# Kernel tuning notes

Measured on AMD Instinct MI355X. Metric: run time of the kernel, lower is better.

## Reference

```python
import jax, jax.numpy as jnp
import numpy as np


def _hippo_dplr(n):
    # HiPPO-LegS -> NPLR -> DPLR (diagonal plus low rank) init, as in S4
    pr = np.sqrt(1.0 + 2.0 * np.arange(n))
    A = -(np.tril(pr[:, None] * pr[None, :]) - np.diag(np.arange(n)))
    p = np.sqrt(np.arange(n) + 0.5)
    b = np.sqrt(2.0 * np.arange(n) + 1.0)
    S = A + p[:, None] * p[None, :]
    lam_re = np.full(n, np.mean(np.diagonal(S)))
    lam_im, V = np.linalg.eigh(S * -1j)  # S*-1j is Hermitian
    p_c = V.conj().T @ p.astype(np.complex128)
    b_c = V.conj().T @ b.astype(np.complex128)
    return lam_re, lam_im, p_c, b_c


def setup_inputs():
    B, L, H, N = 4, 1024, 512, 64
    key = jax.random.key(0)
    kx, kc, ks, k1, k2 = jax.random.split(key, 5)
    lam_re, lam_im, p_c, b_c = _hippo_dplr(N)
    c = jax.random.normal(kc, (N, 2)) * (0.5 ** 0.5)
    f32 = lambda a: jnp.asarray(a, dtype=jnp.float32)
    return {
        'x': jax.random.normal(kx, (B, L, H), dtype=jnp.float32),
        'norm_weight': jnp.ones((H,), jnp.float32),
        'norm_bias': jnp.zeros((H,), jnp.float32),
        'lambda_re': f32(lam_re), 'lambda_im': f32(lam_im),
        'p_re': f32(p_c.real), 'p_im': f32(p_c.imag),
        'b_re': f32(b_c.real), 'b_im': f32(b_c.imag),
        'c_re': c[:, 0].astype(jnp.float32), 'c_im': c[:, 1].astype(jnp.float32),
        'd': jnp.ones((), jnp.float32),
        'log_step': jax.random.uniform(ks, (), jnp.float32, float(np.log(0.001)), float(np.log(0.1))),
        'out_w': (jax.random.normal(k1, (H, H), jnp.float32) / np.sqrt(H)).astype(jnp.float32),
        'out_b': jnp.zeros((H,), jnp.float32),
        'out2_w': (jax.random.normal(k2, (H, H), jnp.float32) / np.sqrt(H)).astype(jnp.float32),
        'out2_b': jnp.zeros((H,), jnp.float32),
    }


def reference(x, norm_weight, norm_bias, lambda_re, lambda_im, p_re, p_im,
              b_re, b_im, c_re, c_im, d, log_step, out_w, out_b, out2_w, out2_b):
    Bsz, L, H = x.shape
    skip = x
    # LayerNorm over channel dim (eps=1e-5, eqx default)
    mu = jnp.mean(x, -1, keepdims=True)
    var = jnp.mean((x - mu) ** 2, -1, keepdims=True)
    xn = (x - mu) / jnp.sqrt(var + 1e-5) * norm_weight + norm_bias
    # --- S4 DPLR bilinear discretization ---
    lam = (lambda_re + 1j * lambda_im).astype(jnp.complex64)
    p = (p_re + 1j * p_im).astype(jnp.complex64)
    b = (b_re + 1j * b_im).astype(jnp.complex64)
    c = (c_re + 1j * c_im).astype(jnp.complex64)
    step = jnp.exp(log_step).astype(jnp.complex64)
    N = lam.shape[0]
    I = jnp.eye(N, dtype=jnp.complex64)
    A = jnp.diag(lam) - p[:, None] * p[None, :].conj()
    A0 = (2.0 / step) * I + A
    Dinv = jnp.diag(1.0 / ((2.0 / step) - lam))
    qcD = p.conj()[None, :] @ Dinv           # [1,N]
    Dp = Dinv @ p[:, None]                   # [N,1]
    A1 = Dinv - (Dp @ qcD) / (1.0 + (qcD @ p[:, None]))  # Woodbury
    Ab = A1 @ A0                             # [N,N] discrete state matrix
    Bb = 2.0 * (A1 @ b[:, None])[:, 0]       # [N]
    # --- sequential state-space scan over time, vectorized over (B,H) lanes ---
    u = xn.astype(jnp.complex64)             # [B,L,H]

    def step_fn(state, u_t):                 # state: [B,H,N], u_t: [B,H]
        new = jnp.einsum('nm,bhm->bhn', Ab, state) + u_t[..., None] * Bb
        return new, jnp.einsum('n,bhn->bh', c, new).real

    init = jnp.zeros((Bsz, H, N), jnp.complex64)
    _, ys = jax.lax.scan(step_fn, init, jnp.moveaxis(u, 1, 0))  # ys: [L,B,H]
    y = jnp.moveaxis(ys, 0, 1) + d * xn      # feedthrough term
    # --- GELU + GLU-style gated output projection, residual ---
    y = jax.nn.gelu(y)
    gate = jax.nn.sigmoid(y @ out2_w.T + out2_b)
    return skip + (y @ out_w.T + out_b) * gate
```

## Files before the change

kernel.cpp:

```cpp
#include <hip/hip_runtime.h>
#include <hip/hip_bf16.h>
#include <math.h>

#define HDIM 512
#define LSEQ 1024
#define BSZ  4

typedef __attribute__((ext_vector_type(8))) short short8;
typedef __attribute__((ext_vector_type(4))) float floatx4;

__device__ __forceinline__ float2 cmul(float2 a, float2 b) {
  float2 r;
  r.x = a.x * b.x - a.y * b.y;
  r.y = a.x * b.y + a.y * b.x;
  return r;
}
__device__ __forceinline__ float2 cadd(float2 a, float2 b) {
  float2 r; r.x = a.x + b.x; r.y = a.y + b.y; return r;
}
__device__ __forceinline__ float2 cfma(float2 a, float2 b, float2 c) {
  c.x += a.x * b.x - a.y * b.y;
  c.y += a.x * b.y + a.y * b.x;
  return c;
}
__device__ __forceinline__ ushort f2bf(float f) {
  __hip_bfloat16 h = __float2bfloat16(f);
  return *(ushort*)&h;
}
__device__ __forceinline__ float bf2f(ushort u) {
  return __bfloat162float(*(__hip_bfloat16*)&u);
}

__global__ __launch_bounds__(576) void stage1_kernel(
    const float* __restrict__ x, const float* __restrict__ nw,
    const float* __restrict__ nb, float* __restrict__ xn,
    const float* __restrict__ lre, const float* __restrict__ lim,
    const float* __restrict__ pre, const float* __restrict__ pim,
    const float* __restrict__ bre, const float* __restrict__ bim,
    const float* __restrict__ cre, const float* __restrict__ cim,
    const float* __restrict__ logstep, float* __restrict__ Kout,
    const float* __restrict__ w1, const float* __restrict__ w2,
    ushort* __restrict__ Wst) {
  __shared__ float2 Ldab[64], Lu[64], Lr[64], LBb[64];
  __shared__ float2 Rv[2048];
  __shared__ float2 Wv[2048];
  int tid = threadIdx.x;
  int wv = tid >> 6;
  int lane = tid & 63;

  if (blockIdx.x != 0) {
    int row = (blockIdx.x - 1) * 9 + wv;
    if (row < BSZ * LSEQ) {
      const float* xr = x + (size_t)row * HDIM;
      float4 v0 = ((const float4*)xr)[lane];
      float4 v1 = ((const float4*)xr)[lane + 64];
      float s  = v0.x + v0.y + v0.z + v0.w + v1.x + v1.y + v1.z + v1.w;
      float ss = v0.x*v0.x + v0.y*v0.y + v0.z*v0.z + v0.w*v0.w
               + v1.x*v1.x + v1.y*v1.y + v1.z*v1.z + v1.w*v1.w;
      #pragma unroll
      for (int m = 1; m < 64; m <<= 1) { s += __shfl_xor(s, m); ss += __shfl_xor(ss, m); }
      float mu   = s * (1.0f / HDIM);
      float var  = ss * (1.0f / HDIM) - mu * mu;
      float rstd = rsqrtf(var + 1e-5f);
      float4 w0 = ((const float4*)nw)[lane];
      float4 w1v = ((const float4*)nw)[lane + 64];
      float4 b0 = ((const float4*)nb)[lane];
      float4 b1 = ((const float4*)nb)[lane + 64];
      float4 o0, o1;
      o0.x = (v0.x - mu) * rstd * w0.x + b0.x;
      o0.y = (v0.y - mu) * rstd * w0.y + b0.y;
      o0.z = (v0.z - mu) * rstd * w0.z + b0.z;
      o0.w = (v0.w - mu) * rstd * w0.w + b0.w;
      o1.x = (v1.x - mu) * rstd * w1v.x + b1.x;
      o1.y = (v1.y - mu) * rstd * w1v.y + b1.y;
      o1.z = (v1.z - mu) * rstd * w1v.z + b1.z;
      o1.w = (v1.w - mu) * rstd * w1v.w + b1.w;
      float* xo = xn + (size_t)row * HDIM;
      ((float4*)xo)[lane] = o0;
      ((float4*)xo)[lane + 64] = o1;
    }
    int idx = (blockIdx.x - 1) * 576 + tid;
    if (idx < 65536) {
      int e0 = idx * 8;
      int n = e0 >> 9, k0 = e0 & 511;
      const float* Wr = (n < 512) ? (w1 + (size_t)n * 512 + k0)
                                  : (w2 + (size_t)(n - 512) * 512 + k0);
      ushort tmp[8];
      #pragma unroll
      for (int q = 0; q < 8; q++) tmp[q] = f2bf(Wr[q]);
      *(short8*)&Wst[e0] = *(short8*)tmp;
    }
    return;
  }

  if (tid < 64) {
    int n = tid;
    float step = expf(logstep[0]);
    float g = 2.0f / step;
    float lr = lre[n], li = lim[n];
    float pr = pre[n], pi = pim[n];
    float br = bre[n], bi = bim[n];
    float den  = (g - lr) * (g - lr) + li * li;
    float dinr = (g - lr) / den, dini = li / den;
    float dabr = (g + lr) * dinr - li * dini;
    float dabi = (g + lr) * dini + li * dinr;
    float ur = dinr * pr - dini * pi;
    float ui = dinr * pi + dini * pr;
    float qr = pr * dinr + pi * dini;
    float qi = pr * dini - pi * dinr;
    float pm2 = pr * pr + pi * pi;
    float betr = pm2 * dinr, beti = pm2 * dini;
    float gar = qr * br - qi * bi;
    float gai = qr * bi + qi * br;
    #pragma unroll
    for (int m = 1; m < 64; m <<= 1) {
      betr += __shfl_xor(betr, m); beti += __shfl_xor(beti, m);
      gar  += __shfl_xor(gar, m);  gai  += __shfl_xor(gai, m);
    }
    float obr = 1.0f + betr, obi = beti;
    float ob2 = obr * obr + obi * obi;
    float kr = -2.0f * g * obr / ob2;
    float ki =  2.0f * g * obi / ob2;
    float rr = kr * qr - ki * qi;
    float ri = kr * qi + ki * qr;
    float tgr = (gar * obr + gai * obi) / ob2;
    float tgi = (gai * obr - gar * obi) / ob2;
    float dbr = dinr * br - dini * bi;
    float dbi = dinr * bi + dini * br;
    float Bbr = 2.0f * (dbr - (ur * tgr - ui * tgi));
    float Bbi = 2.0f * (dbi - (ur * tgi + ui * tgr));
    float2 t;
    t.x = dabr; t.y = dabi; Ldab[n] = t;
    t.x = ur;   t.y = ui;   Lu[n]   = t;
    t.x = rr;   t.y = ri;   Lr[n]   = t;
    t.x = Bbr;  t.y = Bbi;  LBb[n]  = t;
  }
  if (wv == 8) { float2 cc; cc.x = cre[lane]; cc.y = cim[lane]; Rv[lane] = cc; }
  __syncthreads();

  int g8 = lane >> 3;
  int q8 = lane & 7;
  int jm = wv * 8 + g8;
  float2 cv[8];

  if (wv < 8) {
    float2 dab[8], u[8], rn[8];
    #pragma unroll
    for (int ii = 0; ii < 8; ii++) {
      int n = q8 * 8 + ii;
      dab[ii] = Ldab[n]; u[ii] = Lu[n]; rn[ii] = Lr[n];
    }
    float2 rj = Lr[jm];
    #pragma unroll
    for (int ii = 0; ii < 8; ii++) {
      int n = q8 * 8 + ii;
      cv[ii] = cmul(u[ii], rj);
      if (n == jm) cv[ii] = cadd(cv[ii], dab[ii]);
    }
    for (int s = 0; s < 31; s++) {
      float2 part; part.x = 0.f; part.y = 0.f;
      #pragma unroll
      for (int ii = 0; ii < 8; ii++) part = cfma(rn[ii], cv[ii], part);
      #pragma unroll
      for (int m = 1; m < 8; m <<= 1) {
        part.x += __shfl_xor(part.x, m);
        part.y += __shfl_xor(part.y, m);
      }
      #pragma unroll
      for (int ii = 0; ii < 8; ii++) {
        float2 nc = cmul(dab[ii], cv[ii]);
        cv[ii] = cfma(u[ii], part, nc);
      }
    }
  } else {
    float2 dab0 = Ldab[lane], u0 = Lu[lane], r0 = Lr[lane];
    float2 w = LBb[lane];
    Wv[lane * 32 + 0] = w;
    for (int b = 1; b < 32; b++) {
      float dr = r0.x * w.x - r0.y * w.y;
      float di = r0.x * w.y + r0.y * w.x;
      #pragma unroll
      for (int m = 1; m < 64; m <<= 1) { dr += __shfl_xor(dr, m); di += __shfl_xor(di, m); }
      float2 nw2;
      nw2.x = dab0.x * w.x - dab0.y * w.y + u0.x * dr - u0.y * di;
      nw2.y = dab0.x * w.y + dab0.y * w.x + u0.x * di + u0.y * dr;
      w = nw2;
      Wv[lane * 32 + b] = w;
    }
  }
  __syncthreads();

  for (int a = 1; a < 32; a++) {
    if (wv < 8) {
      float2 part; part.x = 0.f; part.y = 0.f;
      #pragma unroll
      for (int ii = 0; ii < 8; ii++) {
        float2 Rk = Rv[(a - 1) * 64 + q8 * 8 + ii];
        part = cfma(Rk, cv[ii], part);
      }
      #pragma unroll
      for (int m = 1; m < 8; m <<= 1) {
        part.x += __shfl_xor(part.x, m);
        part.y += __shfl_xor(part.y, m);
      }
      if (q8 == 0) Rv[a * 64 + jm] = part;
    }
    __syncthreads();
  }

  for (int midx = tid; midx < 1024; midx += 576) {
    int a = midx >> 5, b = midx & 31;
    float acc = 0.f;
    for (int n = 0; n < 64; n++) {
      float2 R = Rv[a * 64 + n];
      float2 W = Wv[n * 32 + b];
      acc += R.x * W.x - R.y * W.y;
    }
    Kout[midx] = acc;
  }
}

__global__ __launch_bounds__(256) void conv_gemm_kernel(
    const float* __restrict__ K, const float* __restrict__ xn,
    const float* __restrict__ dptr, __hip_bfloat16* __restrict__ A) {
  __shared__ ushort sbuf[2 * 7680];
  int tid = threadIdx.x;
  int lane = tid & 63;
  int wv = tid >> 6;
  int wm = wv >> 1, wn = wv & 1;
  int by = blockIdx.y;
  int bm = (by < 8) ? by : 23 - by;
  int bn = blockIdx.x;
  floatx4 acc[2][2] = {};
  int srow = tid >> 2;
  int scol = (tid & 3) * 8;
  int ldst = srow * 40 + scol;
  int fr = lane & 15, fq = (lane >> 4) * 8;
  int trow = bm * 64 + srow;
  int tbase = trow - scol;
  int c = bn * 64 + srow;
  const float* xrow = xn + ((size_t)(c >> 9) * LSEQ) * HDIM + (c & 511);
  int KT = 2 * (bm + 1);

  float tv[8], uv[8];
  #pragma unroll
  for (int i = 0; i < 8; i++) {
    int idx = tbase - i;
    tv[i] = (idx >= 0) ? K[idx] : 0.f;
    uv[i] = xrow[(size_t)(scol + i) * HDIM];
  }
  {
    ushort th[8], tl[8], uu[8];
    #pragma unroll
    for (int i = 0; i < 8; i++) {
      th[i] = f2bf(tv[i]);
      tl[i] = f2bf(tv[i] - bf2f(th[i]));
      uu[i] = f2bf(uv[i]);
    }
    *(short8*)&sbuf[ldst]        = *(short8*)th;
    *(short8*)&sbuf[ldst + 2560] = *(short8*)tl;
    *(short8*)&sbuf[ldst + 5120] = *(short8*)uu;
  }
  __syncthreads();
  for (int kt = 0; kt < KT; kt++) {
    int cur = kt & 1;
    if (kt + 1 < KT) {
      int k0 = (kt + 1) * 32;
      #pragma unroll
      for (int i = 0; i < 8; i++) {
        int idx = tbase - k0 - i;
        tv[i] = (idx >= 0) ? K[idx] : 0.f;
        uv[i] = xrow[(size_t)(k0 + scol + i) * HDIM];
      }
    }
    const ushort* sTh = sbuf + cur * 7680;
    const ushort* sTl = sTh + 2560;
    const ushort* sUh = sTh + 5120;
    short8 ah[2], al[2], bh[2];
    #pragma unroll
    for (int i = 0; i < 2; i++) {
      ah[i] = *(const short8*)&sTh[(wm * 32 + i * 16 + fr) * 40 + fq];
      al[i] = *(const short8*)&sTl[(wm * 32 + i * 16 + fr) * 40 + fq];
      bh[i] = *(const short8*)&sUh[(wn * 32 + i * 16 + fr) * 40 + fq];
    }
    #pragma unroll
    for (int i = 0; i < 2; i++)
      #pragma unroll
      for (int j = 0; j < 2; j++) {
        acc[i][j] = __builtin_amdgcn_mfma_f32_16x16x32_bf16(ah[i], bh[j], acc[i][j], 0, 0, 0);
        acc[i][j] = __builtin_amdgcn_mfma_f32_16x16x32_bf16(al[i], bh[j], acc[i][j], 0, 0, 0);
      }
    if (kt + 1 < KT) {
      ushort th[8], tl[8], uu[8];
      #pragma unroll
      for (int i = 0; i < 8; i++) {
        th[i] = f2bf(tv[i]);
        tl[i] = f2bf(tv[i] - bf2f(th[i]));
        uu[i] = f2bf(uv[i]);
      }
      ushort* dst = sbuf + (cur ^ 1) * 7680;
      *(short8*)&dst[ldst]        = *(short8*)th;
      *(short8*)&dst[ldst + 2560] = *(short8*)tl;
      *(short8*)&dst[ldst + 5120] = *(short8*)uu;
      __syncthreads();
    }
  }
  float d = dptr[0];
  int row0 = bm * 64 + wm * 32;
  int col0 = bn * 64 + wn * 32;
  int fc = lane & 15, frq = (lane >> 4) * 4;
  #pragma unroll
  for (int i = 0; i < 2; i++)
    #pragma unroll
    for (int j = 0; j < 2; j++)
      #pragma unroll
      for (int r = 0; r < 4; r++) {
        int t = row0 + i * 16 + frq + r;
        int cc = col0 + j * 16 + fc;
        int b = cc >> 9, h = cc & 511;
        size_t off = (size_t)(b * LSEQ + t) * HDIM + h;
        float y = acc[i][j][r] + d * xn[off];
        float tnh = tanhf(0.7978845608028654f * (y + 0.044715f * y * y * y));
        A[off] = __float2bfloat16(0.5f * y * (1.0f + tnh));
      }
}

__global__ __launch_bounds__(256) void proj_kernel(
    const __hip_bfloat16* __restrict__ Abuf, const ushort* __restrict__ Wst,
    const float* __restrict__ x, const float* __restrict__ ob,
    const float* __restrict__ o2b, float* __restrict__ out) {
  __shared__ ushort sbuf[2 * 7680];
  int tid = threadIdx.x;
  int lane = tid & 63;
  int wv = tid >> 6;
  int wm = wv >> 1, wn = wv & 1;
  int bm = blockIdx.y, bn = blockIdx.x;
  int srow = tid >> 2;
  int scol = (tid & 3) * 8;
  int ldst = srow * 40 + scol;
  int fr = lane & 15, fq = (lane >> 4) * 8;
  floatx4 acc1[2][2] = {}, acc2[2][2] = {};
  const ushort* Ab = (const ushort*)Abuf;
  size_t Aoff  = (size_t)(bm * 64 + srow) * 512 + scol;
  size_t W1off = (size_t)(bn * 64 + srow) * 512 + scol;
  size_t W2off = W1off + (size_t)512 * 512;
  {
    uint4 a0 = *(const uint4*)&Ab[Aoff];
    uint4 v1 = *(const uint4*)&Wst[W1off];
    uint4 v2 = *(const uint4*)&Wst[W2off];
    *(uint4*)&sbuf[ldst]        = a0;
    *(uint4*)&sbuf[ldst + 2560] = v1;
    *(uint4*)&sbuf[ldst + 5120] = v2;
  }
  __syncthreads();
  for (int kt = 0; kt < 16; kt++) {
    int cur = kt & 1;
    uint4 na = {}, n1 = {}, n2 = {};
    if (kt + 1 < 16) {
      int k1 = (kt + 1) * 32;
      na = *(const uint4*)&Ab[Aoff + k1];
      n1 = *(const uint4*)&Wst[W1off + k1];
      n2 = *(const uint4*)&Wst[W2off + k1];
    }
    const ushort* sA  = sbuf + cur * 7680;
    const ushort* sW1 = sA + 2560;
    const ushort* sW2 = sA + 5120;
    short8 af[2], b1[2], b2[2];
    #pragma unroll
    for (int i = 0; i < 2; i++) {
      af[i] = *(const short8*)&sA[(wm * 32 + i * 16 + fr) * 40 + fq];
      b1[i] = *(const short8*)&sW1[(wn * 32 + i * 16 + fr) * 40 + fq];
      b2[i] = *(const short8*)&sW2[(wn * 32 + i * 16 + fr) * 40 + fq];
    }
    #pragma unroll
    for (int i = 0; i < 2; i++)
      #pragma unroll
      for (int j = 0; j < 2; j++) {
        acc1[i][j] = __builtin_amdgcn_mfma_f32_16x16x32_bf16(af[i], b1[j], acc1[i][j], 0, 0, 0);
        acc2[i][j] = __builtin_amdgcn_mfma_f32_16x16x32_bf16(af[i], b2[j], acc2[i][j], 0, 0, 0);
      }
    if (kt + 1 < 16) {
      ushort* dst = sbuf + (cur ^ 1) * 7680;
      *(uint4*)&dst[ldst]        = na;
      *(uint4*)&dst[ldst + 2560] = n1;
      *(uint4*)&dst[ldst + 5120] = n2;
      __syncthreads();
    }
  }
  int row0 = bm * 64 + wm * 32;
  int col0 = bn * 64 + wn * 32;
  int fc = lane & 15, frq = (lane >> 4) * 4;
  #pragma unroll
  for (int i = 0; i < 2; i++)
    #pragma unroll
    for (int j = 0; j < 2; j++)
      #pragma unroll
      for (int r = 0; r < 4; r++) {
        int row = row0 + i * 16 + frq + r;
        int col = col0 + j * 16 + fc;
        float c1 = acc1[i][j][r] + ob[col];
        float c2 = acc2[i][j][r] + o2b[col];
        float gate = 1.0f / (1.0f + expf(-c2));
        size_t off = (size_t)row * HDIM + col;
        out[off] = x[off] + c1 * gate;
      }
}

extern "C" void kernel_launch(void* const* d_in, const int* in_sizes, int n_in,
                              void* d_out, int out_size, void* d_ws, size_t ws_size,
                              hipStream_t stream) {
  const float* x   = (const float*)d_in[0];
  const float* nw  = (const float*)d_in[1];
  const float* nb  = (const float*)d_in[2];
  const float* lre = (const float*)d_in[3];
  const float* lim = (const float*)d_in[4];
  const float* pre = (const float*)d_in[5];
  const float* pim = (const float*)d_in[6];
  const float* bre = (const float*)d_in[7];
  const float* bim = (const float*)d_in[8];
  const float* cre = (const float*)d_in[9];
  const float* cim = (const float*)d_in[10];
  const float* dsc = (const float*)d_in[11];
  const float* lst = (const float*)d_in[12];
  const float* w1  = (const float*)d_in[13];
  const float* ob  = (const float*)d_in[14];
  const float* w2  = (const float*)d_in[15];
  const float* o2b = (const float*)d_in[16];

  char* ws = (char*)d_ws;
  float* xn    = (float*)(ws);
  ushort* Wst  = (ushort*)(ws + (size_t)(8 << 20));
  __hip_bfloat16* Abuf = (__hip_bfloat16*)(ws + (size_t)(9 << 20));
  float* Kbuf  = (float*)(ws + (size_t)(13 << 20));
  float* out   = (float*)d_out;

  stage1_kernel<<<dim3(457), dim3(576), 0, stream>>>(x, nw, nb, xn,
                                                     lre, lim, pre, pim, bre, bim,
                                                     cre, cim, lst, Kbuf,
                                                     w1, w2, Wst);
  conv_gemm_kernel<<<dim3(32, 16), dim3(256), 0, stream>>>(Kbuf, xn, dsc, Abuf);
  proj_kernel<<<dim3(8, 64), dim3(256), 0, stream>>>(Abuf, Wst, x, ob, o2b, out);
}
```

Measured before the change: 180.0 us.

## Pre-transpose normalized input to bf16 channel-major layout for conv GEMM

The LayerNorm stage now also writes a bf16 copy of the normalized input, transposed to [B*H, L] order through a shared-memory tile. The conv GEMM then loads its B operand with one 16-byte vector load per thread instead of eight strided fp32 loads plus conversions. Weight conversion moves to dedicated blocks, and the LN blocks each handle 64 rows. This removes uncoalesced, heavily repeated strided reads in the GEMM, at the cost of an extra transpose pass and a 4 MB buffer written in stage 1.

```diff
diff --git a/kernel.cpp b/kernel.cpp
--- a/kernel.cpp
+++ b/kernel.cpp
@@ -40,17 +40,34 @@
     const float* __restrict__ cre, const float* __restrict__ cim,
     const float* __restrict__ logstep, float* __restrict__ Kout,
     const float* __restrict__ w1, const float* __restrict__ w2,
-    ushort* __restrict__ Wst) {
+    ushort* __restrict__ Wst, ushort* __restrict__ Uhi) {
   __shared__ float2 Ldab[64], Lu[64], Lr[64], LBb[64];
   __shared__ float2 Rv[2048];
   __shared__ float2 Wv[2048];
+  __shared__ float tile[64][65];
   int tid = threadIdx.x;
   int wv = tid >> 6;
   int lane = tid & 63;
 
+  if (blockIdx.x >= 65) {
+    int idx = (blockIdx.x - 65) * 576 + tid;
+    if (idx < 65536) {
+      int e0 = idx * 8;
+      int n = e0 >> 9, k0 = e0 & 511;
+      const float* Wr = (n < 512) ? (w1 + (size_t)n * 512 + k0)
+                                  : (w2 + (size_t)(n - 512) * 512 + k0);
+      ushort tmp[8];
+      #pragma unroll
+      for (int q = 0; q < 8; q++) tmp[q] = f2bf(Wr[q]);
+      *(short8*)&Wst[e0] = *(short8*)tmp;
+    }
+    return;
+  }
+
   if (blockIdx.x != 0) {
-    int row = (blockIdx.x - 1) * 9 + wv;
-    if (row < BSZ * LSEQ) {
+    int row0 = (blockIdx.x - 1) * 64;
+    for (int r = wv; r < 64; r += 9) {
+      int row = row0 + r;
       const float* xr = x + (size_t)row * HDIM;
       float4 v0 = ((const float4*)xr)[lane];
       float4 v1 = ((const float4*)xr)[lane + 64];
@@ -79,16 +96,23 @@
       ((float4*)xo)[lane] = o0;
       ((float4*)xo)[lane + 64] = o1;
     }
-    int idx = (blockIdx.x - 1) * 576 + tid;
-    if (idx < 65536) {
-      int e0 = idx * 8;
-      int n = e0 >> 9, k0 = e0 & 511;
-      const float* Wr = (n < 512) ? (w1 + (size_t)n * 512 + k0)
-                                  : (w2 + (size_t)(n - 512) * 512 + k0);
-      ushort tmp[8];
-      #pragma unroll
-      for (int q = 0; q < 8; q++) tmp[q] = f2bf(Wr[q]);
-      *(short8*)&Wst[e0] = *(short8*)tmp;
+    __syncthreads();
+    int b = row0 >> 10, t0 = row0 & 1023;
+    for (int hc = 0; hc < 8; hc++) {
+      for (int e = tid; e < 4096; e += 576) {
+        int r = e >> 6, cc = e & 63;
+        tile[r][cc] = xn[(size_t)(row0 + r) * HDIM + hc * 64 + cc];
+      }
+      __syncthreads();
+      if (tid < 512) {
+        int h = tid >> 3, tt = (tid & 7) * 8;
+        ushort tmp[8];
+        #pragma unroll
+        for (int i = 0; i < 8; i++) tmp[i] = f2bf(tile[tt + i][h]);
+        *(short8*)&Uhi[((size_t)(b * 512 + hc * 64 + h)) * 1024 + t0 + tt] =
+            *(short8*)tmp;
+      }
+      __syncthreads();
     }
     return;
   }
@@ -221,8 +245,9 @@
 }
 
 __global__ __launch_bounds__(256) void conv_gemm_kernel(
-    const float* __restrict__ K, const float* __restrict__ xn,
-    const float* __restrict__ dptr, __hip_bfloat16* __restrict__ A) {
+    const float* __restrict__ K, const ushort* __restrict__ Uhi,
+    const float* __restrict__ xn, const float* __restrict__ dptr,
+    __hip_bfloat16* __restrict__ A) {
   __shared__ ushort sbuf[2 * 7680];
   int tid = threadIdx.x;
   int lane = tid & 63;
@@ -236,42 +261,41 @@
   int scol = (tid & 3) * 8;
   int ldst = srow * 40 + scol;
   int fr = lane & 15, fq = (lane >> 4) * 8;
-  int trow = bm * 64 + srow;
-  int tbase = trow - scol;
-  int c = bn * 64 + srow;
-  const float* xrow = xn + ((size_t)(c >> 9) * LSEQ) * HDIM + (c & 511);
+  int tbase = bm * 64 + srow - scol;
+  size_t Uoff = (size_t)(bn * 64 + srow) * 1024 + scol;
   int KT = 2 * (bm + 1);
 
-  float tv[8], uv[8];
-  #pragma unroll
-  for (int i = 0; i < 8; i++) {
-    int idx = tbase - i;
-    tv[i] = (idx >= 0) ? K[idx] : 0.f;
-    uv[i] = xrow[(size_t)(scol + i) * HDIM];
-  }
   {
-    ushort th[8], tl[8], uu[8];
+    float tv[8];
+    #pragma unroll
+    for (int i = 0; i < 8; i++) {
+      int idx = tbase - i;
+      tv[i] = (idx >= 0) ? K[idx] : 0.f;
+    }
+    uint4 uh = *(const uint4*)&Uhi[Uoff];
+    ushort th[8], tl[8];
     #pragma unroll
     for (int i = 0; i < 8; i++) {
       th[i] = f2bf(tv[i]);
       tl[i] = f2bf(tv[i] - bf2f(th[i]));
-      uu[i] = f2bf(uv[i]);
     }
     *(short8*)&sbuf[ldst]        = *(short8*)th;
     *(short8*)&sbuf[ldst + 2560] = *(short8*)tl;
-    *(short8*)&sbuf[ldst + 5120] = *(short8*)uu;
+    *(uint4*)&sbuf[ldst + 5120]  = uh;
   }
   __syncthreads();
   for (int kt = 0; kt < KT; kt++) {
     int cur = kt & 1;
+    float tv[8];
+    uint4 nuh = {};
     if (kt + 1 < KT) {
       int k0 = (kt + 1) * 32;
       #pragma unroll
       for (int i = 0; i < 8; i++) {
         int idx = tbase - k0 - i;
         tv[i] = (idx >= 0) ? K[idx] : 0.f;
-        uv[i] = xrow[(size_t)(k0 + scol + i) * HDIM];
-      }
+      }
+      nuh = *(const uint4*)&Uhi[Uoff + k0];
     }
     const ushort* sTh = sbuf + cur * 7680;
     const ushort* sTl = sTh + 2560;
@@ -291,17 +315,16 @@
         acc[i][j] = __builtin_amdgcn_mfma_f32_16x16x32_bf16(al[i], bh[j], acc[i][j], 0, 0, 0);
       }
     if (kt + 1 < KT) {
-      ushort th[8], tl[8], uu[8];
+      ushort th[8], tl[8];
       #pragma unroll
       for (int i = 0; i < 8; i++) {
         th[i] = f2bf(tv[i]);
         tl[i] = f2bf(tv[i] - bf2f(th[i]));
-        uu[i] = f2bf(uv[i]);
       }
       ushort* dst = sbuf + (cur ^ 1) * 7680;
       *(short8*)&dst[ldst]        = *(short8*)th;
       *(short8*)&dst[ldst + 2560] = *(short8*)tl;
-      *(short8*)&dst[ldst + 5120] = *(short8*)uu;
+      *(uint4*)&dst[ldst + 5120]  = nuh;
       __syncthreads();
     }
   }
@@ -429,15 +452,16 @@
 
   char* ws = (char*)d_ws;
   float* xn    = (float*)(ws);
-  ushort* Wst  = (ushort*)(ws + (size_t)(8 << 20));
-  __hip_bfloat16* Abuf = (__hip_bfloat16*)(ws + (size_t)(9 << 20));
-  float* Kbuf  = (float*)(ws + (size_t)(13 << 20));
+  ushort* Uhi  = (ushort*)(ws + (size_t)(8  << 20));
+  ushort* Wst  = (ushort*)(ws + (size_t)(12 << 20));
+  __hip_bfloat16* Abuf = (__hip_bfloat16*)(ws + (size_t)(13 << 20));
+  float* Kbuf  = (float*)(ws + (size_t)(17 << 20));
   float* out   = (float*)d_out;
 
-  stage1_kernel<<<dim3(457), dim3(576), 0, stream>>>(x, nw, nb, xn,
+  stage1_kernel<<<dim3(179), dim3(576), 0, stream>>>(x, nw, nb, xn,
                                                      lre, lim, pre, pim, bre, bim,
                                                      cre, cim, lst, Kbuf,
-                                                     w1, w2, Wst);
-  conv_gemm_kernel<<<dim3(32, 16), dim3(256), 0, stream>>>(Kbuf, xn, dsc, Abuf);
+                                                     w1, w2, Wst, Uhi);
+  conv_gemm_kernel<<<dim3(32, 16), dim3(256), 0, stream>>>(Kbuf, Uhi, xn, dsc, Abuf);
   proj_kernel<<<dim3(8, 64), dim3(256), 0, stream>>>(Abuf, Wst, x, ob, o2b, out);
 }
```

New measurement: 166.7 us. 1.08x faster.
